# Kernel optimization log

Hardware: AMD Instinct MI355X
Metric: run time of the kernel (lower is better)

The kernel has to match this reference:

```python
import jax, jax.numpy as jnp
import numpy as np

EPS = 1e-7  # keras K.epsilon()
ROUTINGS = 3


def squash(v, axis=-1):
    s = jnp.sum(v * v, axis=axis, keepdims=True)
    scale = s / (1.0 + s) / jnp.sqrt(s + EPS)
    return scale * v


def setup_inputs() -> dict:
    key = jax.random.key(0)
    k1, k2 = jax.random.split(key)
    B, I, K = 256, 2048, 8   # batch, input_num_capsule, input_dim_capsule
    J, D = 10, 16            # num_capsule, dim_capsule
    inputs = jax.random.normal(k1, (B, I, K), dtype=jnp.float32)
    W = jax.random.normal(k2, (J, I, D, K), dtype=jnp.float32) * 0.05
    return {"inputs": inputs, "W": W}


def reference(inputs, W):
    # inputs: [B, I, K]; W: [J, I, D, K]
    # inputs_hat[b,j,i,d] = W[j,i] @ inputs[b,i]  -> [B, J, I, D]
    u_hat = jnp.einsum('jidk,bik->bjid', W, inputs)
    B, J, I, _ = u_hat.shape
    b = jnp.zeros((B, J, 1, I), dtype=u_hat.dtype)
    outputs = None
    for r in range(ROUTINGS):
        c = jax.nn.softmax(b, axis=1)                       # softmax over output capsules
        s = jnp.einsum('bjqi,bjid->bjqd', c, u_hat)          # [B, J, 1, D]
        outputs = squash(s, axis=-1)
        if r < ROUTINGS - 1:
            b = b + jnp.einsum('bjqd,bjid->bjqi', outputs, u_hat)
    return jnp.squeeze(outputs, axis=2)                      # [B, J, D]
```

## Files before the change

kernel.cpp:

```cpp
#include <hip/hip_runtime.h>
#include <math.h>


#define BB 256
#define II 2048
#define KK 8
#define JJ 10
#define DD 16

typedef __attribute__((ext_vector_type(4))) float f32x4;
typedef __attribute__((ext_vector_type(8))) short short8;

__device__ __forceinline__ short f2bf(float f) {
    union { float f; unsigned u; } v; v.f = f;
    unsigned r = v.u + 0x7FFFu + ((v.u >> 16) & 1u);
    return (short)(r >> 16);
}

__device__ __forceinline__ void gload16(const short* g, short* l) {
    __builtin_amdgcn_global_load_lds(
        (const __attribute__((address_space(1))) unsigned int*)g,
        (__attribute__((address_space(3))) unsigned int*)l,
        16, 0, 0);
}

#define LBUF 14336

__device__ __forceinline__ void seg_src_dst(int s, int i0, int b0,
                                            const short* __restrict__ xTb,
                                            const short* __restrict__ Wb,
                                            const short** src, int* dst) {
    if (s < 20) {
        const int j = s >> 1, h = s & 1;
        *src = Wb + ((size_t)(j * II + i0) * DD) * KK + h * 512;
        *dst = j * 1024 + h * 512;
    } else {
        const int il = s - 20;
        *src = xTb + ((size_t)(i0 + il) * BB + b0) * KK;
        *dst = 10240 + il * 512;
    }
}

__global__ __launch_bounds__(256) void round1_fused(
    const float* __restrict__ x, const float* __restrict__ W,
    short* __restrict__ xTb, short* __restrict__ Wb, _Float16* __restrict__ p)
{
    __shared__ short L[2][LBUF];
    const int t = threadIdx.x;
    const int lane = t & 63, wv = t >> 6;
    const int col = lane & 15, q = lane >> 4;
    const int chunk = blockIdx.x, ytile = blockIdx.y;
    const int b0 = ytile * 64;
    const int bl = wv * 16 + col;
    const int i0 = chunk * 16;

#pragma unroll
    for (int n = 0; n < 10; ++n) {
        const int r = t + n * 256;
        const int d = r & 15, i = (r >> 4) & 15, j = r >> 8;
        const size_t off = ((size_t)(j * II + i0 + i) * DD + d) * KK;
        const float4 a = *(const float4*)(W + off);
        const float4 b = *(const float4*)(W + off + 4);
        short8 o;
        o[0] = f2bf(a.x); o[1] = f2bf(a.y); o[2] = f2bf(a.z); o[3] = f2bf(a.w);
        o[4] = f2bf(b.x); o[5] = f2bf(b.y); o[6] = f2bf(b.z); o[7] = f2bf(b.w);
        *(short8*)(&L[i >> 3][j * 1024 + (i & 7) * 128 + d * 8]) = o;
        if (ytile == 0) *(short8*)(Wb + off) = o;
    }
#pragma unroll
    for (int n = 0; n < 4; ++n) {
        const int r = t + n * 256;
        const int b = r & 63, i = r >> 6;
        const float* xp = x + ((size_t)(b0 + b) * II + (i0 + i)) * KK;
        const float4 a = *(const float4*)xp;
        const float4 c = *(const float4*)(xp + 4);
        short8 o;
        o[0] = f2bf(a.x); o[1] = f2bf(a.y); o[2] = f2bf(a.z); o[3] = f2bf(a.w);
        o[4] = f2bf(c.x); o[5] = f2bf(c.y); o[6] = f2bf(c.z); o[7] = f2bf(c.w);
        *(short8*)(&L[i >> 3][10240 + (i & 7) * 512 + b * 8]) = o;
        *(short8*)(xTb + ((size_t)(i0 + i) * BB + b0 + b) * KK) = o;
    }
    __syncthreads();

    f32x4 sfrag[JJ];
#pragma unroll
    for (int j = 0; j < JJ; ++j) sfrag[j] = (f32x4){0.f, 0.f, 0.f, 0.f};

#pragma unroll
    for (int sc = 0; sc < 2; ++sc) {
        const short* Lb = L[sc];
#pragma unroll
        for (int s = 0; s < 2; ++s) {
            const int il = s * 4 + q;
            const short8 Bf = *(const short8*)(&Lb[10240 + il * 512 + bl * 8]);
#pragma unroll
            for (int j = 0; j < JJ; ++j) {
                const short8 A = *(const short8*)(&Lb[j * 1024 + il * 128 + col * 8]);
                sfrag[j] = __builtin_amdgcn_mfma_f32_16x16x32_bf16(A, Bf, sfrag[j], 0, 0, 0);
            }
        }
    }

    _Float16* pp = p + ((size_t)(ytile * 4 + wv) * 128 + chunk) * (JJ * 256);
#pragma unroll
    for (int j = 0; j < JJ; ++j) {
        union { uint2 u; _Float16 h[4]; } pk;
        pk.h[0] = (_Float16)sfrag[j][0];
        pk.h[1] = (_Float16)sfrag[j][1];
        pk.h[2] = (_Float16)sfrag[j][2];
        pk.h[3] = (_Float16)sfrag[j][3];
        *(uint2*)(pp + (size_t)(j * 64 + lane) * 4) = pk.u;
    }
}

__global__ __launch_bounds__(256) void round_mfma(
    const short* __restrict__ xTb, const short* __restrict__ Wb,
    const float* __restrict__ vT, _Float16* __restrict__ p)
{
    __shared__ short L[2][LBUF];
    const int t = threadIdx.x;
    const int lane = t & 63, wv = t >> 6;
    const int col = lane & 15, q = lane >> 4;
    const int b0 = blockIdx.y * 64;
    const int bl = wv * 16 + col;
    const int i0 = blockIdx.x * 16;

#pragma unroll
    for (int n = 0; n < 7; ++n) {
        const int s = wv + n * 4;
        const short* src; int dst;
        seg_src_dst(s, i0, b0, xTb, Wb, &src, &dst);
        gload16(src + lane * 8, &L[0][dst]);
        seg_src_dst(s, i0 + 8, b0, xTb, Wb, &src, &dst);
        gload16(src + lane * 8, &L[1][dst]);
    }

    float vfrag[JJ][4];
#pragma unroll
    for (int j = 0; j < JJ; ++j)
#pragma unroll
        for (int r = 0; r < 4; ++r)
            vfrag[j][r] = vT[(j * DD + q * 4 + r) * BB + b0 + bl];

    __syncthreads();

    f32x4 sfrag[JJ];
#pragma unroll
    for (int j = 0; j < JJ; ++j) sfrag[j] = (f32x4){0.f, 0.f, 0.f, 0.f};

#pragma unroll
    for (int sc = 0; sc < 2; ++sc) {
        const short* Lb = L[sc];
#pragma unroll 2
        for (int il = 0; il < 8; ++il) {
            short8 A[JJ], Bf;
            const short8 z = (short8){0, 0, 0, 0, 0, 0, 0, 0};
            Bf = z;
#pragma unroll
            for (int j = 0; j < JJ; ++j) A[j] = z;
            if (q == 0) {
                Bf = *(const short8*)(&Lb[10240 + il * 512 + bl * 8]);
#pragma unroll
                for (int j = 0; j < JJ; ++j)
                    A[j] = *(const short8*)(&Lb[j * 1024 + il * 128 + col * 8]);
            }
            f32x4 U[JJ];
#pragma unroll
            for (int j = 0; j < JJ; ++j)
                U[j] = __builtin_amdgcn_mfma_f32_16x16x32_bf16(
                    A[j], Bf, (f32x4){0.f, 0.f, 0.f, 0.f}, 0, 0, 0);
            float Lg[JJ];
#pragma unroll
            for (int j = 0; j < JJ; ++j)
                Lg[j] = vfrag[j][0] * U[j][0] + vfrag[j][1] * U[j][1]
                      + vfrag[j][2] * U[j][2] + vfrag[j][3] * U[j][3];
#pragma unroll
            for (int j = 0; j < JJ; ++j) {
                Lg[j] += __shfl_xor(Lg[j], 16, 64);
                Lg[j] += __shfl_xor(Lg[j], 32, 64);
            }
            float sum = 0.f;
#pragma unroll
            for (int j = 0; j < JJ; ++j) { Lg[j] = __expf(Lg[j]); sum += Lg[j]; }
            const float inv = __builtin_amdgcn_rcpf(sum);
#pragma unroll
            for (int j = 0; j < JJ; ++j) {
                const float c = Lg[j] * inv;
#pragma unroll
                for (int r = 0; r < 4; ++r) sfrag[j][r] += c * U[j][r];
            }
        }
    }

    _Float16* pp = p + ((size_t)(blockIdx.y * 4 + wv) * 128 + blockIdx.x) * (JJ * 256);
#pragma unroll
    for (int j = 0; j < JJ; ++j) {
        union { uint2 u; _Float16 h[4]; } pk;
        pk.h[0] = (_Float16)sfrag[j][0];
        pk.h[1] = (_Float16)sfrag[j][1];
        pk.h[2] = (_Float16)sfrag[j][2];
        pk.h[3] = (_Float16)sfrag[j][3];
        *(uint2*)(pp + (size_t)(j * 64 + lane) * 4) = pk.u;
    }
}

template <int MODE>
__global__ __launch_bounds__(512) void rs_kernel(const _Float16* __restrict__ p,
                                                 float* __restrict__ vT,
                                                 float* __restrict__ out, float scale) {
    __shared__ f32x4 red[512];
    const int t = threadIdx.x;
    const int j = blockIdx.x, bt = blockIdx.y;
    const int eg = t & 63, cg = t >> 6;

    const _Float16* pp = p + ((size_t)bt * 128 + cg * 16) * (JJ * 256) + j * 256 + eg * 4;
    float s0 = 0.f, s1 = 0.f, s2 = 0.f, s3 = 0.f;
#pragma unroll 8
    for (int ch = 0; ch < 16; ++ch) {
        union { uint2 u; _Float16 h[4]; } cv;
        cv.u = *(const uint2*)(pp + (size_t)ch * (JJ * 256));
        s0 += (float)cv.h[0]; s1 += (float)cv.h[1];
        s2 += (float)cv.h[2]; s3 += (float)cv.h[3];
    }
    red[t] = (f32x4){s0, s1, s2, s3};
    __syncthreads();
    if (t < 64) {
        f32x4 a = red[t];
#pragma unroll
        for (int g = 1; g < 8; ++g) a += red[64 * g + t];
        const float x0 = a[0] * scale, x1 = a[1] * scale;
        const float x2 = a[2] * scale, x3 = a[3] * scale;
        float ss = x0 * x0 + x1 * x1 + x2 * x2 + x3 * x3;
        ss += __shfl_xor(ss, 16, 64);
        ss += __shfl_xor(ss, 32, 64);
        const float coef = ss / (1.f + ss) / sqrtf(ss + 1e-7f);
        const int qd = t >> 4, bc = t & 15;
        const float v[4] = {coef * x0, coef * x1, coef * x2, coef * x3};
#pragma unroll
        for (int r = 0; r < 4; ++r) {
            const int d = qd * 4 + r;
            if (MODE == 0) vT[(j * DD + d) * BB + bt * 16 + bc] = v[r];
            if (MODE == 1) vT[(j * DD + d) * BB + bt * 16 + bc] += v[r];
            if (MODE == 2) out[((bt * 16 + bc) * JJ + j) * DD + d] = v[r];
        }
    }
}

#define IT_OLD 32
#define BT_OLD 16

__global__ __launch_bounds__(256) void zero_kernel(float* __restrict__ p, int n) {
    int idx = blockIdx.x * blockDim.x + threadIdx.x;
    if (idx < n) p[idx] = 0.f;
}

__global__ __launch_bounds__(256) void squash_old(float* __restrict__ s_acc,
                                                  float* __restrict__ dst, float scale,
                                                  int add_to_dst, int zero_src) {
    int idx = blockIdx.x * blockDim.x + threadIdx.x;
    if (idx >= BB * JJ) return;
    float s[DD];
    float ss = 0.f;
#pragma unroll
    for (int d = 0; d < DD; ++d) {
        s[d] = s_acc[idx * DD + d] * scale;
        ss += s[d] * s[d];
    }
    const float coef = ss / (1.f + ss) / sqrtf(ss + 1e-7f);
#pragma unroll
    for (int d = 0; d < DD; ++d) {
        const float vv = coef * s[d];
        if (add_to_dst) dst[idx * DD + d] += vv;
        else            dst[idx * DD + d] = vv;
        if (zero_src)   s_acc[idx * DD + d] = 0.f;
    }
}

__global__ __launch_bounds__(256) void round1_old(const float* __restrict__ x,
                                                  const float* __restrict__ W,
                                                  float* __restrict__ s_acc) {
    const int t = threadIdx.x;
    const int d = t & 15;
    const int bq = t >> 4;
    const int b = blockIdx.y * BT_OLD + bq;
    const int i0 = blockIdx.x * IT_OLD;
    float acc[JJ];
#pragma unroll
    for (int j = 0; j < JJ; ++j) acc[j] = 0.f;
    for (int ii = 0; ii < IT_OLD; ++ii) {
        const int i = i0 + ii;
        const float* xp = x + ((b * II) + i) * KK;
        const float4 xa = *(const float4*)(xp);
        const float4 xb = *(const float4*)(xp + 4);
#pragma unroll
        for (int j = 0; j < JJ; ++j) {
            const float* wp = W + (((j * II + i) * DD + d) * KK);
            const float4 w0 = *(const float4*)(wp);
            const float4 w1 = *(const float4*)(wp + 4);
            acc[j] += w0.x*xa.x + w0.y*xa.y + w0.z*xa.z + w0.w*xa.w
                    + w1.x*xb.x + w1.y*xb.y + w1.z*xb.z + w1.w*xb.w;
        }
    }
#pragma unroll
    for (int j = 0; j < JJ; ++j)
        atomicAdd(&s_acc[(b * JJ + j) * DD + d], acc[j]);
}

__global__ __launch_bounds__(256) void round_old(const float* __restrict__ x,
                                                 const float* __restrict__ W,
                                                 const float* __restrict__ v,
                                                 float* __restrict__ s_acc) {
    const int t = threadIdx.x;
    const int d = t & 15;
    const int bq = t >> 4;
    const int b = blockIdx.y * BT_OLD + bq;
    const int i0 = blockIdx.x * IT_OLD;
    float vr[JJ], acc[JJ];
#pragma unroll
    for (int j = 0; j < JJ; ++j) {
        vr[j] = v[(b * JJ + j) * DD + d];
        acc[j] = 0.f;
    }
    for (int ii = 0; ii < IT_OLD; ++ii) {
        const int i = i0 + ii;
        const float* xp = x + ((b * II) + i) * KK;
        const float4 xa = *(const float4*)(xp);
        const float4 xb = *(const float4*)(xp + 4);
        float U[JJ], Lg[JJ];
#pragma unroll
        for (int j = 0; j < JJ; ++j) {
            const float* wp = W + (((j * II + i) * DD + d) * KK);
            const float4 w0 = *(const float4*)(wp);
            const float4 w1 = *(const float4*)(wp + 4);
            U[j] = w0.x*xa.x + w0.y*xa.y + w0.z*xa.z + w0.w*xa.w
                 + w1.x*xb.x + w1.y*xb.y + w1.z*xb.z + w1.w*xb.w;
            Lg[j] = vr[j] * U[j];
        }
#pragma unroll
        for (int m = 8; m >= 1; m >>= 1) {
#pragma unroll
            for (int j = 0; j < JJ; ++j) Lg[j] += __shfl_xor(Lg[j], m, 64);
        }
        float mx = Lg[0];
#pragma unroll
        for (int j = 1; j < JJ; ++j) mx = fmaxf(mx, Lg[j]);
        float sum = 0.f;
#pragma unroll
        for (int j = 0; j < JJ; ++j) { Lg[j] = __expf(Lg[j] - mx); sum += Lg[j]; }
        const float inv = 1.f / sum;
#pragma unroll
        for (int j = 0; j < JJ; ++j) acc[j] += (Lg[j] * inv) * U[j];
    }
#pragma unroll
    for (int j = 0; j < JJ; ++j)
        atomicAdd(&s_acc[(b * JJ + j) * DD + d], acc[j]);
}

extern "C" void kernel_launch(void* const* d_in, const int* in_sizes, int n_in,
                              void* d_out, int out_size, void* d_ws, size_t ws_size,
                              hipStream_t stream) {
    const float* x = (const float*)d_in[0];
    const float* W = (const float*)d_in[1];
    float* out = (float*)d_out;

    float* vT     = (float*)d_ws;
    _Float16* p   = (_Float16*)(vT + BB * JJ * DD);
    short* xTb    = (short*)(p + (size_t)16 * 128 * 2560);
    short* Wb     = xTb + (size_t)II * BB * KK;
    const size_t need = (size_t)(BB * JJ * DD) * 4
                      + (size_t)16 * 128 * 2560 * 2
                      + ((size_t)II * BB * KK + (size_t)JJ * II * DD * KK) * 2;

    if (ws_size >= need) {
        dim3 rg(128, 4);
        dim3 sg(JJ, 16);
        round1_fused<<<rg, 256, 0, stream>>>(x, W, xTb, Wb, p);
        rs_kernel<0><<<sg, 512, 0, stream>>>(p, vT, out, 0.1f);
        round_mfma<<<rg, 256, 0, stream>>>(xTb, Wb, vT, p);
        rs_kernel<1><<<sg, 512, 0, stream>>>(p, vT, out, 1.0f);
        round_mfma<<<rg, 256, 0, stream>>>(xTb, Wb, vT, p);
        rs_kernel<2><<<sg, 512, 0, stream>>>(p, vT, out, 1.0f);
    } else {
        float* s_acc = (float*)d_ws;
        float* v_buf = s_acc + BB * JJ * DD;
        const int NS = BB * JJ * DD;
        dim3 rg(II / IT_OLD, BB / BT_OLD);
        zero_kernel<<<(NS + 255) / 256, 256, 0, stream>>>(s_acc, NS);
        round1_old<<<rg, 256, 0, stream>>>(x, W, s_acc);
        squash_old<<<(BB * JJ + 255) / 256, 256, 0, stream>>>(s_acc, v_buf, 0.1f, 0, 1);
        round_old<<<rg, 256, 0, stream>>>(x, W, v_buf, s_acc);
        squash_old<<<(BB * JJ + 255) / 256, 256, 0, stream>>>(s_acc, v_buf, 1.0f, 1, 1);
        round_old<<<rg, 256, 0, stream>>>(x, W, v_buf, s_acc);
        squash_old<<<(BB * JJ + 255) / 256, 256, 0, stream>>>(s_acc, out, 1.0f, 0, 0);
    }
}
```

Measured before the change: 136.8 us.

## Replace partial-sum buffers and reduce kernels with atomic accumulation and fused squash

Each routing round now accumulates its per-block partial sums straight into fp32 global accumulators with atomicAdd. This replaces writing fp16 partials to a large buffer and reducing them in separate rs_kernel launches. The squash of earlier rounds is recomputed inside the next round's prologue from the raw accumulators, and a small squash_out kernel produces the final output. This removes two kernel launches and the partial-buffer traffic, but adds a memset, a large number of contended atomics (128 chunks per address), and redundant squash work in every block.

```diff
diff --git a/kernel.cpp b/kernel.cpp
--- a/kernel.cpp
+++ b/kernel.cpp
@@ -43,7 +43,7 @@
 
 __global__ __launch_bounds__(256) void round1_fused(
     const float* __restrict__ x, const float* __restrict__ W,
-    short* __restrict__ xTb, short* __restrict__ Wb, _Float16* __restrict__ p)
+    short* __restrict__ xTb, short* __restrict__ Wb, float* __restrict__ s0)
 {
     __shared__ short L[2][LBUF];
     const int t = threadIdx.x;
@@ -101,21 +101,18 @@
         }
     }
 
-    _Float16* pp = p + ((size_t)(ytile * 4 + wv) * 128 + chunk) * (JJ * 256);
-#pragma unroll
-    for (int j = 0; j < JJ; ++j) {
-        union { uint2 u; _Float16 h[4]; } pk;
-        pk.h[0] = (_Float16)sfrag[j][0];
-        pk.h[1] = (_Float16)sfrag[j][1];
-        pk.h[2] = (_Float16)sfrag[j][2];
-        pk.h[3] = (_Float16)sfrag[j][3];
-        *(uint2*)(pp + (size_t)(j * 64 + lane) * 4) = pk.u;
-    }
-}
-
+#pragma unroll
+    for (int j = 0; j < JJ; ++j)
+#pragma unroll
+        for (int r = 0; r < 4; ++r)
+            atomicAdd(&s0[(j * DD + q * 4 + r) * BB + b0 + bl], sfrag[j][r]);
+}
+
+template <int RND>
 __global__ __launch_bounds__(256) void round_mfma(
     const short* __restrict__ xTb, const short* __restrict__ Wb,
-    const float* __restrict__ vT, _Float16* __restrict__ p)
+    const float* __restrict__ s0, const float* __restrict__ s1,
+    float* __restrict__ sd)
 {
     __shared__ short L[2][LBUF];
     const int t = threadIdx.x;
@@ -136,11 +133,38 @@
     }
 
     float vfrag[JJ][4];
-#pragma unroll
-    for (int j = 0; j < JJ; ++j)
-#pragma unroll
-        for (int r = 0; r < 4; ++r)
-            vfrag[j][r] = vT[(j * DD + q * 4 + r) * BB + b0 + bl];
+    {
+        const int bcol = b0 + bl;
+#pragma unroll
+        for (int j = 0; j < JJ; ++j) {
+            float x0[4];
+            float ssp = 0.f;
+#pragma unroll
+            for (int r = 0; r < 4; ++r) {
+                x0[r] = 0.1f * s0[(j * DD + q * 4 + r) * BB + bcol];
+                ssp += x0[r] * x0[r];
+            }
+            ssp += __shfl_xor(ssp, 16, 64);
+            ssp += __shfl_xor(ssp, 32, 64);
+            const float c0 = ssp / (1.f + ssp) / sqrtf(ssp + 1e-7f);
+#pragma unroll
+            for (int r = 0; r < 4; ++r) vfrag[j][r] = c0 * x0[r];
+            if (RND == 3) {
+                float x1[4];
+                float ss1 = 0.f;
+#pragma unroll
+                for (int r = 0; r < 4; ++r) {
+                    x1[r] = s1[(j * DD + q * 4 + r) * BB + bcol];
+                    ss1 += x1[r] * x1[r];
+                }
+                ss1 += __shfl_xor(ss1, 16, 64);
+                ss1 += __shfl_xor(ss1, 32, 64);
+                const float c1 = ss1 / (1.f + ss1) / sqrtf(ss1 + 1e-7f);
+#pragma unroll
+                for (int r = 0; r < 4; ++r) vfrag[j][r] += c1 * x1[r];
+            }
+        }
+    }
 
     __syncthreads();
 
@@ -192,58 +216,27 @@
         }
     }
 
-    _Float16* pp = p + ((size_t)(blockIdx.y * 4 + wv) * 128 + blockIdx.x) * (JJ * 256);
-#pragma unroll
-    for (int j = 0; j < JJ; ++j) {
-        union { uint2 u; _Float16 h[4]; } pk;
-        pk.h[0] = (_Float16)sfrag[j][0];
-        pk.h[1] = (_Float16)sfrag[j][1];
-        pk.h[2] = (_Float16)sfrag[j][2];
-        pk.h[3] = (_Float16)sfrag[j][3];
-        *(uint2*)(pp + (size_t)(j * 64 + lane) * 4) = pk.u;
-    }
-}
-
-template <int MODE>
-__global__ __launch_bounds__(512) void rs_kernel(const _Float16* __restrict__ p,
-                                                 float* __restrict__ vT,
-                                                 float* __restrict__ out, float scale) {
-    __shared__ f32x4 red[512];
-    const int t = threadIdx.x;
-    const int j = blockIdx.x, bt = blockIdx.y;
-    const int eg = t & 63, cg = t >> 6;
-
-    const _Float16* pp = p + ((size_t)bt * 128 + cg * 16) * (JJ * 256) + j * 256 + eg * 4;
-    float s0 = 0.f, s1 = 0.f, s2 = 0.f, s3 = 0.f;
-#pragma unroll 8
-    for (int ch = 0; ch < 16; ++ch) {
-        union { uint2 u; _Float16 h[4]; } cv;
-        cv.u = *(const uint2*)(pp + (size_t)ch * (JJ * 256));
-        s0 += (float)cv.h[0]; s1 += (float)cv.h[1];
-        s2 += (float)cv.h[2]; s3 += (float)cv.h[3];
-    }
-    red[t] = (f32x4){s0, s1, s2, s3};
-    __syncthreads();
-    if (t < 64) {
-        f32x4 a = red[t];
-#pragma unroll
-        for (int g = 1; g < 8; ++g) a += red[64 * g + t];
-        const float x0 = a[0] * scale, x1 = a[1] * scale;
-        const float x2 = a[2] * scale, x3 = a[3] * scale;
-        float ss = x0 * x0 + x1 * x1 + x2 * x2 + x3 * x3;
-        ss += __shfl_xor(ss, 16, 64);
-        ss += __shfl_xor(ss, 32, 64);
-        const float coef = ss / (1.f + ss) / sqrtf(ss + 1e-7f);
-        const int qd = t >> 4, bc = t & 15;
-        const float v[4] = {coef * x0, coef * x1, coef * x2, coef * x3};
-#pragma unroll
-        for (int r = 0; r < 4; ++r) {
-            const int d = qd * 4 + r;
-            if (MODE == 0) vT[(j * DD + d) * BB + bt * 16 + bc] = v[r];
-            if (MODE == 1) vT[(j * DD + d) * BB + bt * 16 + bc] += v[r];
-            if (MODE == 2) out[((bt * 16 + bc) * JJ + j) * DD + d] = v[r];
-        }
-    }
+#pragma unroll
+    for (int j = 0; j < JJ; ++j)
+#pragma unroll
+        for (int r = 0; r < 4; ++r)
+            atomicAdd(&sd[(j * DD + q * 4 + r) * BB + b0 + bl], sfrag[j][r]);
+}
+
+__global__ __launch_bounds__(256) void squash_out(const float* __restrict__ s2,
+                                                  float* __restrict__ out) {
+    const int j = blockIdx.x, b = threadIdx.x;
+    float xv[DD];
+    float ss = 0.f;
+#pragma unroll
+    for (int d = 0; d < DD; ++d) {
+        xv[d] = s2[(j * DD + d) * BB + b];
+        ss += xv[d] * xv[d];
+    }
+    const float coef = ss / (1.f + ss) / sqrtf(ss + 1e-7f);
+#pragma unroll
+    for (int d = 0; d < DD; ++d)
+        out[((size_t)b * JJ + j) * DD + d] = coef * xv[d];
 }
 
 #define IT_OLD 32
@@ -363,34 +356,34 @@
     const float* W = (const float*)d_in[1];
     float* out = (float*)d_out;
 
-    float* vT     = (float*)d_ws;
-    _Float16* p   = (_Float16*)(vT + BB * JJ * DD);
-    short* xTb    = (short*)(p + (size_t)16 * 128 * 2560);
+    float* s_acc  = (float*)d_ws;
+    short* xTb    = (short*)(s_acc + 3 * BB * JJ * DD);
     short* Wb     = xTb + (size_t)II * BB * KK;
-    const size_t need = (size_t)(BB * JJ * DD) * 4
-                      + (size_t)16 * 128 * 2560 * 2
+    const size_t need = (size_t)3 * BB * JJ * DD * 4
                       + ((size_t)II * BB * KK + (size_t)JJ * II * DD * KK) * 2;
 
     if (ws_size >= need) {
+        float* s0 = s_acc;
+        float* s1 = s_acc + BB * JJ * DD;
+        float* s2 = s_acc + 2 * BB * JJ * DD;
+        hipMemsetAsync(s_acc, 0, (size_t)3 * BB * JJ * DD * 4, stream);
+
         dim3 rg(128, 4);
-        dim3 sg(JJ, 16);
-        round1_fused<<<rg, 256, 0, stream>>>(x, W, xTb, Wb, p);
-        rs_kernel<0><<<sg, 512, 0, stream>>>(p, vT, out, 0.1f);
-        round_mfma<<<rg, 256, 0, stream>>>(xTb, Wb, vT, p);
-        rs_kernel<1><<<sg, 512, 0, stream>>>(p, vT, out, 1.0f);
-        round_mfma<<<rg, 256, 0, stream>>>(xTb, Wb, vT, p);
-        rs_kernel<2><<<sg, 512, 0, stream>>>(p, vT, out, 1.0f);
+        round1_fused<<<rg, 256, 0, stream>>>(x, W, xTb, Wb, s0);
+        round_mfma<2><<<rg, 256, 0, stream>>>(xTb, Wb, s0, s0, s1);
+        round_mfma<3><<<rg, 256, 0, stream>>>(xTb, Wb, s0, s1, s2);
+        squash_out<<<JJ, 256, 0, stream>>>(s2, out);
     } else {
-        float* s_acc = (float*)d_ws;
-        float* v_buf = s_acc + BB * JJ * DD;
+        float* sacc  = (float*)d_ws;
+        float* v_buf = sacc + BB * JJ * DD;
         const int NS = BB * JJ * DD;
         dim3 rg(II / IT_OLD, BB / BT_OLD);
-        zero_kernel<<<(NS + 255) / 256, 256, 0, stream>>>(s_acc, NS);
-        round1_old<<<rg, 256, 0, stream>>>(x, W, s_acc);
-        squash_old<<<(BB * JJ + 255) / 256, 256, 0, stream>>>(s_acc, v_buf, 0.1f, 0, 1);
-        round_old<<<rg, 256, 0, stream>>>(x, W, v_buf, s_acc);
-        squash_old<<<(BB * JJ + 255) / 256, 256, 0, stream>>>(s_acc, v_buf, 1.0f, 1, 1);
-        round_old<<<rg, 256, 0, stream>>>(x, W, v_buf, s_acc);
-        squash_old<<<(BB * JJ + 255) / 256, 256, 0, stream>>>(s_acc, out, 1.0f, 0, 0);
-    }
-}
+        zero_kernel<<<(NS + 255) / 256, 256, 0, stream>>>(sacc, NS);
+        round1_old<<<rg, 256, 0, stream>>>(x, W, sacc);
+        squash_old<<<(BB * JJ + 255) / 256, 256, 0, stream>>>(sacc, v_buf, 0.1f, 0, 1);
+        round_old<<<rg, 256, 0, stream>>>(x, W, v_buf, sacc);
+        squash_old<<<(BB * JJ + 255) / 256, 256, 0, stream>>>(sacc, v_buf, 1.0f, 1, 1);
+        round_old<<<rg, 256, 0, stream>>>(x, W, v_buf, sacc);
+        squash_old<<<(BB * JJ + 255) / 256, 256, 0, stream>>>(sacc, out, 1.0f, 0, 0);
+    }
+}
```

New measurement: 206.2 us. 50.8% more time.
